# Kernel tuning notes

Hardware: AMD Instinct MI355X
Metric: run time of the kernel (lower is better)

The kernel has to match this reference:

```python
import jax, jax.numpy as jnp
import numpy as np

NUM_HEADS = 16
INNER = 128      # per-head q/k dim
OUT = 128        # per-head v dim
D_MODEL = 1024
SEQ = 2048
MASK_SCALE = -1000000000.0  # ENSURE_MASKED_IS_ZERO


def setup_inputs() -> dict:
    key = jax.random.key(0)
    ks = jax.random.split(key, 8)
    scale = 1.0 / np.sqrt(D_MODEL)
    inputs = jax.random.normal(ks[0], (SEQ, D_MODEL), dtype=jnp.float32)
    sequence_mask = jax.random.bernoulli(ks[1], 0.5, (SEQ,))
    Wq = jax.random.normal(ks[2], (D_MODEL, NUM_HEADS * INNER), dtype=jnp.float32) * scale
    bq = jnp.zeros((NUM_HEADS * INNER,), dtype=jnp.float32)
    Wk = jax.random.normal(ks[3], (D_MODEL, NUM_HEADS * INNER), dtype=jnp.float32) * scale
    bk = jnp.zeros((NUM_HEADS * INNER,), dtype=jnp.float32)
    Wv = jax.random.normal(ks[4], (D_MODEL, NUM_HEADS * OUT), dtype=jnp.float32) * scale
    bv = jnp.zeros((NUM_HEADS * OUT,), dtype=jnp.float32)
    return {"inputs": inputs, "sequence_mask": sequence_mask,
            "Wq": Wq, "bq": bq, "Wk": Wk, "bk": bk, "Wv": Wv, "bv": bv}


def reference(inputs, sequence_mask, Wq, bq, Wk, bk, Wv, bv):
    S = inputs.shape[0]
    # Dense projections, then split heads; vmap(in_axes=1) in the original == head-major layout [H, S, D]
    q = (inputs @ Wq + bq).reshape(S, NUM_HEADS, INNER).transpose(1, 0, 2)
    k = (inputs @ Wk + bk).reshape(S, NUM_HEADS, INNER).transpose(1, 0, 2)
    v = (inputs @ Wv + bv).reshape(S, NUM_HEADS, OUT).transpose(1, 0, 2)
    # raw scores / sqrt(d_k)
    scores = jnp.einsum('hsd,htd->hst', q, k) / jnp.sqrt(jnp.float32(INNER))
    # Faithful to original: scores are MULTIPLIED by the mask matrix
    # mask = outer(m, m) * (-1e9): -1e9 where both positions True, 0 otherwise.
    mask = (sequence_mask[:, None] & sequence_mask[None, :]).astype(scores.dtype) * MASK_SCALE
    scores = scores * mask  # broadcast over head axis
    attn = jax.nn.softmax(scores, axis=-1)           # [H, S, S]
    out = jnp.einsum('hst,htd->hsd', attn, v)        # [H, S, OUT]
    return out.transpose(1, 0, 2).reshape(S, NUM_HEADS * OUT)
```

## Files before the change

### kernel.cpp

```cpp
#include <hip/hip_runtime.h>
#include <hip/hip_bf16.h>
#include <cfloat>
#include <math.h>

typedef __bf16 bf16;
typedef __bf16 bf16x4 __attribute__((ext_vector_type(4)));
typedef __bf16 bf16x8 __attribute__((ext_vector_type(8)));
typedef float  floatx4 __attribute__((ext_vector_type(4)));
typedef float  floatx2 __attribute__((ext_vector_type(2)));

#define SEQ 2048
#define DM  1024
#define NP  2048
#define CAP (1 << 20)
#define MARGIN 0.5f
#define LBUF 1024

__device__ __forceinline__ unsigned enc_f(float f) {
  unsigned b = __float_as_uint(f);
  return ((int)b >= 0) ? (b | 0x80000000u) : ~b;
}
__device__ __forceinline__ float dec_f(unsigned u) {
  return (u & 0x80000000u) ? __uint_as_float(u & 0x7fffffffu) : __uint_as_float(~u);
}

__global__ __launch_bounds__(256) void mask_prep(
    const void* __restrict__ mraw, int* __restrict__ maskw,
    int* __restrict__ midx, int* __restrict__ mc,
    int* __restrict__ gcount, float* __restrict__ sums,
    unsigned long long* __restrict__ keys, unsigned* __restrict__ gmin) {
  int t = threadIdx.x;
  if (blockIdx.x > 0) {
    int b = blockIdx.x - 1;
    for (int j = 0; j < 4; j++) {
      int i = b * 1024 + j * 256 + t;
      keys[i] = ~0ULL;
      gmin[i] = 0xFFFFFFFFu;
    }
    if (b == 0) for (int i = t; i < 2048; i += 256) sums[i] = 0.f;
    return;
  }
  __shared__ int flags;
  __shared__ int lmask[2048];
  if (t == 0) { flags = 0; *gcount = 0; }
  __syncthreads();
  const unsigned short* u16 = (const unsigned short*)mraw;
  const unsigned* u32 = (const unsigned*)mraw;
  int f = 0;
  for (int i = t; i < 1024; i += 256) {
    unsigned short v = u16[i];
    if (v != 0 && v != 0x3F80u) f |= 1;
    if ((i & 1) == 0 && v == 0x3F80u) f |= 2;
  }
  for (int i = t; i < 512; i += 256)
    if (u32[i] > 1u) f |= 4;
  if (f) atomicOr(&flags, f);
  __syncthreads();
  int fl = flags;
  int mode;
  if (!(fl & 1)) mode = (fl & 2) ? 2 : 3;
  else           mode = (fl & 4) ? 1 : 0;
  for (int s = t; s < SEQ; s += 256) {
    int m;
    if (mode == 0)      m = (((const int*)mraw)[s] != 0);
    else if (mode == 1) m = (((const unsigned char*)mraw)[s] != 0);
    else if (mode == 2) m = (u16[s] != 0);
    else                m = (((const float*)mraw)[s] != 0.0f);
    maskw[s] = m; lmask[s] = m;
  }
  __syncthreads();
  if (t < 64) {
    int base = 0;
    for (int c = 0; c < 32; c++) {
      int s = c * 64 + t;
      bool m = lmask[s] != 0;
      unsigned long long bal = __ballot(m);
      if (m) midx[base + __popcll(bal & ((1ULL << t) - 1ULL))] = s;
      base += __popcll(bal);
    }
    if (t == 0) *mc = base;
  }
}

__global__ __launch_bounds__(256) void split_x(
    const float* __restrict__ X,
    bf16* __restrict__ Xh, bf16* __restrict__ Xm) {
  int i = blockIdx.x * 256 + threadIdx.x;
  floatx4 v = *(const floatx4*)(X + (size_t)i * 4);
  bf16x4 hv, mv;
  #pragma unroll
  for (int j = 0; j < 4; j++) {
    float x = v[j];
    bf16 h = (bf16)x; float r1 = x - (float)h;
    hv[j] = h; mv[j] = (bf16)r1;
  }
  *(bf16x4*)(Xh + (size_t)i * 4) = hv;
  *(bf16x4*)(Xm + (size_t)i * 4) = mv;
}

__global__ __launch_bounds__(256) void split_w(
    const float* __restrict__ Wq, const float* __restrict__ Wk,
    const float* __restrict__ Wv,
    bf16* __restrict__ Tqh, bf16* __restrict__ Tqm,
    bf16* __restrict__ Tkh, bf16* __restrict__ Tkm,
    bf16* __restrict__ Tvh) {
  int z = blockIdx.z;
  const float* W = (z == 0) ? Wq : (z == 1) ? Wk : Wv;
  bf16* Th = (z == 0) ? Tqh : (z == 1) ? Tkh : Tvh;
  bf16* Tm = (z == 0) ? Tqm : Tkm;
  __shared__ float tile[32][33];
  int n0 = blockIdx.x * 32, k0 = blockIdx.y * 32;
  int t = threadIdx.x, r = t >> 3, c4 = (t & 7) * 4;
  floatx4 v = *(const floatx4*)(W + (size_t)(k0 + r) * NP + n0 + c4);
  tile[r][c4 + 0] = v[0]; tile[r][c4 + 1] = v[1];
  tile[r][c4 + 2] = v[2]; tile[r][c4 + 3] = v[3];
  __syncthreads();
  bf16x4 hv, mv;
  #pragma unroll
  for (int j = 0; j < 4; j++) {
    float x = tile[c4 + j][r];
    bf16 h = (bf16)x; float r1 = x - (float)h;
    hv[j] = h; mv[j] = (bf16)r1;
  }
  size_t base = (size_t)(n0 + r) * DM + k0 + c4;
  *(bf16x4*)(Th + base) = hv;
  if (z < 2)
    *(bf16x4*)(Tm + base) = mv;
}

__global__ __launch_bounds__(256) void proj_qk3(
    const bf16* __restrict__ Xh, const bf16* __restrict__ Xm,
    const bf16* __restrict__ Qh_, const bf16* __restrict__ Qm_,
    const bf16* __restrict__ Kh_, const bf16* __restrict__ Km_,
    const float* __restrict__ bq, const float* __restrict__ bk,
    const int* __restrict__ midx, const int* __restrict__ mc,
    float* __restrict__ qf, float* __restrict__ kf,
    bf16* __restrict__ qbf, bf16* __restrict__ kbf) {
  int mcv = *mc;
  int lin = blockIdx.x;
  int z    = lin & 1;
  int head = (lin >> 1) & 15;
  int ms   = (lin >> 5) * 64;
  if (mcv == 0 || ms >= mcv) return;
  const bf16* WTh = z ? Kh_ : Qh_;
  const bf16* WTm = z ? Km_ : Qm_;
  const float* bia = z ? bk : bq;
  float* outf = z ? kf : qf;
  bf16*  outb = z ? kbf : qbf;
  int ns = head * 128;
  __shared__ alignas(16) bf16 Ah[64][40], Am[64][40];
  __shared__ alignas(16) bf16 Bh[128][40], Bm[128][40];
  int t = threadIdx.x, w = t >> 6, lane = t & 63, l15 = lane & 15, qd = lane >> 4;
  int wm = (w & 1) * 32, wn = (w >> 1) * 64;
  int amr = t >> 2, akb = (t & 3) * 8;
  int bnr = t >> 1, bkb = (t & 1) * 16;
  int cr = ms + amr;
  size_t arow = (size_t)midx[cr < mcv ? cr : (mcv - 1)] * DM + akb;
  const bf16* xhp = Xh + arow;
  const bf16* xmp = Xm + arow;
  const bf16* bhp = WTh + (size_t)(ns + bnr) * DM + bkb;
  const bf16* bmp = WTm + (size_t)(ns + bnr) * DM + bkb;

  floatx4 acc[2][4];
  for (int i = 0; i < 2; i++)
    for (int j = 0; j < 4; j++) acc[i][j] = (floatx4){0.f, 0.f, 0.f, 0.f};

  bf16x8 pa[2], pb[4];
  pa[0] = *(const bf16x8*)(xhp);
  pa[1] = *(const bf16x8*)(xmp);
  pb[0] = *(const bf16x8*)(bhp);     pb[1] = *(const bf16x8*)(bhp + 8);
  pb[2] = *(const bf16x8*)(bmp);     pb[3] = *(const bf16x8*)(bmp + 8);

  for (int kt = 0; kt < DM; kt += 32) {
    __syncthreads();
    *(bf16x8*)&Ah[amr][akb] = pa[0];
    *(bf16x8*)&Am[amr][akb] = pa[1];
    *(bf16x8*)&Bh[bnr][bkb]     = pb[0];
    *(bf16x8*)&Bh[bnr][bkb + 8] = pb[1];
    *(bf16x8*)&Bm[bnr][bkb]     = pb[2];
    *(bf16x8*)&Bm[bnr][bkb + 8] = pb[3];
    __syncthreads();
    if (kt + 32 < DM) {
      int k2 = kt + 32;
      pa[0] = *(const bf16x8*)(xhp + k2);
      pa[1] = *(const bf16x8*)(xmp + k2);
      pb[0] = *(const bf16x8*)(bhp + k2);     pb[1] = *(const bf16x8*)(bhp + k2 + 8);
      pb[2] = *(const bf16x8*)(bmp + k2);     pb[3] = *(const bf16x8*)(bmp + k2 + 8);
    }
    bf16x8 fah[2], fam[2], fbh[4], fbm[4];
    #pragma unroll
    for (int i = 0; i < 2; i++) {
      fah[i] = *(const bf16x8*)&Ah[wm + i * 16 + l15][qd * 8];
      fam[i] = *(const bf16x8*)&Am[wm + i * 16 + l15][qd * 8];
    }
    #pragma unroll
    for (int j = 0; j < 4; j++) {
      fbh[j] = *(const bf16x8*)&Bh[wn + j * 16 + l15][qd * 8];
      fbm[j] = *(const bf16x8*)&Bm[wn + j * 16 + l15][qd * 8];
    }
    #pragma unroll
    for (int i = 0; i < 2; i++)
      #pragma unroll
      for (int j = 0; j < 4; j++) {
        floatx4 a = acc[i][j];
        a = __builtin_amdgcn_mfma_f32_16x16x32_bf16(fam[i], fbh[j], a, 0, 0, 0);
        a = __builtin_amdgcn_mfma_f32_16x16x32_bf16(fah[i], fbm[j], a, 0, 0, 0);
        a = __builtin_amdgcn_mfma_f32_16x16x32_bf16(fah[i], fbh[j], a, 0, 0, 0);
        acc[i][j] = a;
      }
  }
  #pragma unroll
  for (int i = 0; i < 2; i++)
    #pragma unroll
    for (int j = 0; j < 4; j++) {
      int col = wn + j * 16 + l15;
      float bb = bia[ns + col];
      #pragma unroll
      for (int r = 0; r < 4; r++) {
        int row = ms + wm + i * 16 + qd * 4 + r;
        float v = acc[i][j][r] + bb;
        size_t idx = ((size_t)head * SEQ + row) * 128 + col;
        outf[idx] = v;
        outb[idx] = (bf16)v;
      }
    }
}

__global__ __launch_bounds__(256) void proj_v_mfma(
    const bf16* __restrict__ Xh, const bf16* __restrict__ Wvh,
    const float* __restrict__ bia, float* __restrict__ out,
    float* __restrict__ sums) {
  __shared__ alignas(16) bf16 As[64][40];
  __shared__ alignas(16) bf16 Bs[128][40];
  __shared__ float colsum[128];
  int lin = blockIdx.x;
  int ns = (lin & 15) * 128;
  int ms = (lin >> 4) * 64;
  int t = threadIdx.x, w = t >> 6, lane = t & 63, l15 = lane & 15, qd = lane >> 4;
  int wm = (w & 1) * 32, wn = (w >> 1) * 64;
  int amr = t >> 2, akb = (t & 3) * 8;
  int bnr = t >> 1, bkb = (t & 1) * 16;
  if (t < 128) colsum[t] = 0.f;
  const bf16* ap = Xh  + (size_t)(ms + amr) * DM + akb;
  const bf16* bp = Wvh + (size_t)(ns + bnr) * DM + bkb;
  floatx4 acc[2][4];
  for (int i = 0; i < 2; i++)
    for (int j = 0; j < 4; j++) acc[i][j] = (floatx4){0.f, 0.f, 0.f, 0.f};

  bf16x8 pa, pb[2];
  pa    = *(const bf16x8*)(ap);
  pb[0] = *(const bf16x8*)(bp);  pb[1] = *(const bf16x8*)(bp + 8);

  for (int kt = 0; kt < DM; kt += 32) {
    __syncthreads();
    *(bf16x8*)&As[amr][akb]     = pa;
    *(bf16x8*)&Bs[bnr][bkb]     = pb[0];
    *(bf16x8*)&Bs[bnr][bkb + 8] = pb[1];
    __syncthreads();
    if (kt + 32 < DM) {
      int k2 = kt + 32;
      pa    = *(const bf16x8*)(ap + k2);
      pb[0] = *(const bf16x8*)(bp + k2);  pb[1] = *(const bf16x8*)(bp + k2 + 8);
    }
    bf16x8 af[2], bfr[4];
    #pragma unroll
    for (int i = 0; i < 2; i++) af[i]  = *(const bf16x8*)&As[wm + i * 16 + l15][qd * 8];
    #pragma unroll
    for (int j = 0; j < 4; j++) bfr[j] = *(const bf16x8*)&Bs[wn + j * 16 + l15][qd * 8];
    #pragma unroll
    for (int i = 0; i < 2; i++)
      #pragma unroll
      for (int j = 0; j < 4; j++)
        acc[i][j] = __builtin_amdgcn_mfma_f32_16x16x32_bf16(af[i], bfr[j], acc[i][j], 0, 0, 0);
  }
  float part[4] = {0.f, 0.f, 0.f, 0.f};
  for (int i = 0; i < 2; i++) {
    for (int j = 0; j < 4; j++) {
      int n = ns + wn + j * 16 + l15;
      float bb = bia[n];
      for (int r = 0; r < 4; r++) {
        int m = ms + wm + i * 16 + qd * 4 + r;
        float v = acc[i][j][r] + bb;
        out[(size_t)m * NP + n] = v;
        part[j] += v;
      }
    }
  }
  for (int j = 0; j < 4; j++)
    atomicAdd(&colsum[wn + j * 16 + l15], part[j]);
  __syncthreads();
  if (t < 128) atomicAdd(&sums[ns + t], colsum[t]);
}

__global__ __launch_bounds__(256) void scores_min(
    const bf16* __restrict__ Qb, const bf16* __restrict__ Kb,
    const int* __restrict__ mc,
    unsigned* __restrict__ gmin) {
  int mcv = *mc;
  int h = blockIdx.x, s0 = blockIdx.y * 64;
  if (s0 >= mcv) return;
  int ntiles = (mcv + 63) >> 6;
  int half = (ntiles + 1) >> 1;
  int tbeg = blockIdx.z * half;
  int tend = ntiles < tbeg + half ? ntiles : tbeg + half;
  if (tbeg >= tend) return;
  __shared__ float lmin[64][4];
  int t = threadIdx.x, w = t >> 6, lane = t & 63, l15 = lane & 15, qd = lane >> 4;
  const bf16* Qh = Qb + (size_t)h * SEQ * 128;
  const bf16* Kh = Kb + (size_t)h * SEQ * 128;
  bf16x8 af[4][4];
  #pragma unroll
  for (int ksp = 0; ksp < 4; ksp++)
    #pragma unroll
    for (int i = 0; i < 4; i++)
      af[ksp][i] = *(const bf16x8*)(Qh + (size_t)(s0 + i * 16 + l15) * 128 + ksp * 32 + qd * 8);
  const bf16* kb = Kh + (size_t)(w * 16 + l15) * 128 + qd * 8;
  float rmin[4][4];
  for (int i = 0; i < 4; i++)
    for (int r = 0; r < 4; r++) rmin[i][r] = INFINITY;
  bf16x8 pre[4];
  #pragma unroll
  for (int ksp = 0; ksp < 4; ksp++)
    pre[ksp] = *(const bf16x8*)(kb + (size_t)tbeg * 8192 + ksp * 32);

  for (int tt = tbeg; tt < tend; tt++) {
    bf16x8 cur[4];
    #pragma unroll
    for (int ksp = 0; ksp < 4; ksp++) cur[ksp] = pre[ksp];
    if (tt + 1 < tend) {
      #pragma unroll
      for (int ksp = 0; ksp < 4; ksp++)
        pre[ksp] = *(const bf16x8*)(kb + (size_t)(tt + 1) * 8192 + ksp * 32);
    }
    floatx4 acc[4];
    for (int i = 0; i < 4; i++) acc[i] = (floatx4){0.f, 0.f, 0.f, 0.f};
    #pragma unroll
    for (int ksp = 0; ksp < 4; ksp++)
      #pragma unroll
      for (int i = 0; i < 4; i++)
        acc[i] = __builtin_amdgcn_mfma_f32_16x16x32_bf16(af[ksp][i], cur[ksp], acc[i], 0, 0, 0);
    bool okc = (tt * 64 + w * 16 + l15) < mcv;
    for (int i = 0; i < 4; i++)
      for (int r = 0; r < 4; r++)
        rmin[i][r] = fminf(rmin[i][r], okc ? acc[i][r] : INFINITY);
  }
  for (int m = 1; m < 16; m <<= 1)
    for (int i = 0; i < 4; i++)
      for (int r = 0; r < 4; r++)
        rmin[i][r] = fminf(rmin[i][r], __shfl_xor(rmin[i][r], m));
  if (l15 == 0)
    for (int i = 0; i < 4; i++)
      for (int r = 0; r < 4; r++)
        lmin[i * 16 + qd * 4 + r][w] = rmin[i][r];
  __syncthreads();
  if (t < 64) {
    int row = s0 + t;
    if (row < mcv) {
      float cm = fminf(fminf(lmin[t][0], lmin[t][1]), fminf(lmin[t][2], lmin[t][3]));
      atomicMin(&gmin[h * 2048 + row], enc_f(cm));
    }
  }
}

__global__ __launch_bounds__(256) void scores_collect(
    const bf16* __restrict__ Qb, const bf16* __restrict__ Kb,
    const int* __restrict__ mc, const unsigned* __restrict__ gmin,
    unsigned* __restrict__ cand, int* __restrict__ gcount) {
  int mcv = *mc;
  int h = blockIdx.x, s0 = blockIdx.y * 64;
  if (s0 >= mcv) return;
  int ntiles = (mcv + 63) >> 6;
  int half = (ntiles + 1) >> 1;
  int tbeg = blockIdx.z * half;
  int tend = ntiles < tbeg + half ? ntiles : tbeg + half;
  if (tbeg >= tend) return;
  __shared__ unsigned lbuf[LBUF];
  __shared__ int lcount;
  __shared__ int gbase;
  int t = threadIdx.x, w = t >> 6, lane = t & 63, l15 = lane & 15, qd = lane >> 4;
  if (t == 0) lcount = 0;
  const bf16* Qh = Qb + (size_t)h * SEQ * 128;
  const bf16* Kh = Kb + (size_t)h * SEQ * 128;
  bf16x8 af[4][4];
  #pragma unroll
  for (int ksp = 0; ksp < 4; ksp++)
    #pragma unroll
    for (int i = 0; i < 4; i++)
      af[ksp][i] = *(const bf16x8*)(Qh + (size_t)(s0 + i * 16 + l15) * 128 + ksp * 32 + qd * 8);
  float fm[4][4];
  for (int i = 0; i < 4; i++)
    for (int r = 0; r < 4; r++) {
      int row = s0 + i * 16 + qd * 4 + r;
      fm[i][r] = (row < mcv) ? dec_f(gmin[h * 2048 + row]) + MARGIN : -INFINITY;
    }
  const bf16* kb = Kh + (size_t)(w * 16 + l15) * 128 + qd * 8;
  bf16x8 pre[4];
  #pragma unroll
  for (int ksp = 0; ksp < 4; ksp++)
    pre[ksp] = *(const bf16x8*)(kb + (size_t)tbeg * 8192 + ksp * 32);
  __syncthreads();

  for (int tt = tbeg; tt < tend; tt++) {
    bf16x8 cur[4];
    #pragma unroll
    for (int ksp = 0; ksp < 4; ksp++) cur[ksp] = pre[ksp];
    if (tt + 1 < tend) {
      #pragma unroll
      for (int ksp = 0; ksp < 4; ksp++)
        pre[ksp] = *(const bf16x8*)(kb + (size_t)(tt + 1) * 8192 + ksp * 32);
    }
    floatx4 acc[4];
    for (int i = 0; i < 4; i++) acc[i] = (floatx4){0.f, 0.f, 0.f, 0.f};
    #pragma unroll
    for (int ksp = 0; ksp < 4; ksp++)
      #pragma unroll
      for (int i = 0; i < 4; i++)
        acc[i] = __builtin_amdgcn_mfma_f32_16x16x32_bf16(af[ksp][i], cur[ksp], acc[i], 0, 0, 0);
    int tg = tt * 64 + w * 16 + l15;
    if (tg < mcv) {
      for (int i = 0; i < 4; i++)
        for (int r = 0; r < 4; r++) {
          if (acc[i][r] <= fm[i][r]) {
            int rr = i * 16 + qd * 4 + r;
            unsigned enc = ((unsigned)h << 22) | ((unsigned)(s0 + rr) << 11) | (unsigned)tg;
            int lp = atomicAdd(&lcount, 1);
            if (lp < LBUF) {
              lbuf[lp] = enc;
            } else {
              int pos = atomicAdd(gcount, 1);
              if (pos < CAP) cand[pos] = enc;
            }
          }
        }
    }
  }
  __syncthreads();
  int cnt = lcount; if (cnt > LBUF) cnt = LBUF;
  if (t == 0) gbase = atomicAdd(gcount, cnt);
  __syncthreads();
  int base = gbase;
  for (int i = t; i < cnt; i += 256) {
    int pos = base + i;
    if (pos < CAP) cand[pos] = lbuf[i];
  }
}

__global__ __launch_bounds__(256) void rescore(
    const float* __restrict__ Q, const float* __restrict__ K,
    const int* __restrict__ midx,
    const unsigned* __restrict__ cand, const int* __restrict__ gcount,
    unsigned long long* __restrict__ keys) {
  int wid  = (blockIdx.x * 256 + threadIdx.x) >> 6;
  int lane = threadIdx.x & 63;
  int nw = gridDim.x * 4;
  int n = *gcount; if (n > CAP) n = CAP;
  for (int c = wid; c < n; c += nw) {
    unsigned u = cand[c];
    int h = u >> 22, cs = (u >> 11) & 2047, ct = u & 2047;
    floatx2 qv = *(const floatx2*)(Q + ((size_t)h * SEQ + cs) * 128 + lane * 2);
    floatx2 kv = *(const floatx2*)(K + ((size_t)h * SEQ + ct) * 128 + lane * 2);
    double d = (double)qv[0] * (double)kv[0] + (double)qv[1] * (double)kv[1];
    for (int off = 32; off; off >>= 1) d += __shfl_down(d, off);
    if (lane == 0) {
      int sorig = midx[cs], torig = midx[ct];
      long long b = __double_as_longlong(d);
      unsigned long long ub = (b >= 0) ? ((unsigned long long)b | 0x8000000000000000ULL)
                                       : ~(unsigned long long)b;
      unsigned long long key = (ub & ~2047ULL) | (unsigned long long)torig;
      atomicMin(&keys[(size_t)h * SEQ + sorig], key);
    }
  }
}

__global__ __launch_bounds__(256) void assemble(
    const float* __restrict__ V, const float* __restrict__ sums,
    const int* __restrict__ mask, const unsigned long long* __restrict__ keys,
    float* __restrict__ out) {
  int idx = blockIdx.x * 256 + threadIdx.x;
  int s = idx >> 11, n = idx & 2047, h = n >> 7;
  float val;
  if (mask[s]) {
    int tt = (int)(keys[(size_t)h * SEQ + s] & 2047ULL);
    val = V[(size_t)tt * NP + n];
  } else {
    val = sums[n] * (1.0f / 2048.0f);
  }
  out[idx] = val;
}

extern "C" void kernel_launch(void* const* d_in, const int* in_sizes, int n_in,
                              void* d_out, int out_size, void* d_ws, size_t ws_size,
                              hipStream_t stream) {
  (void)in_sizes; (void)n_in; (void)out_size; (void)ws_size;
  const float* X    = (const float*)d_in[0];
  const void*  mraw = d_in[1];
  const float* Wq   = (const float*)d_in[2];
  const float* bq   = (const float*)d_in[3];
  const float* Wk   = (const float*)d_in[4];
  const float* bk   = (const float*)d_in[5];
  const float* Wv   = (const float*)d_in[6];
  const float* bv   = (const float*)d_in[7];

  char* ws = (char*)d_ws;
  float* qf  = (float*)ws;
  float* kf  = (float*)(ws + ((size_t)16 << 20));
  bf16*  qbf = (bf16*) (ws + ((size_t)32 << 20));
  bf16*  kbf = (bf16*) (ws + ((size_t)40 << 20));
  bf16* wqh = (bf16*)(ws + ((size_t)48 << 20));
  bf16* wqm = (bf16*)(ws + ((size_t)52 << 20));
  bf16* wkh = (bf16*)(ws + ((size_t)56 << 20));
  bf16* wkm = (bf16*)(ws + ((size_t)60 << 20));
  float* vf = (float*)(ws + ((size_t)48 << 20));
  unsigned* cand = (unsigned*)(ws + ((size_t)64 << 20));
  char* misc = ws + ((size_t)72 << 20);
  int*   maskw  = (int*)misc;
  int*   midx   = (int*)(misc + (8 << 10));
  int*   mc     = (int*)(misc + (16 << 10));
  int*   gcount = (int*)(misc + (16 << 10) + 64);
  float* sums   = (float*)(misc + (32 << 10));
  unsigned long long* keys = (unsigned long long*)(misc + (64 << 10));
  unsigned* gmin = (unsigned*)(misc + (320 << 10));
  bf16* xh  = (bf16*)(ws + ((size_t)73 << 20));
  bf16* xm  = (bf16*)(ws + ((size_t)77 << 20));
  bf16* tvh = (bf16*)(ws + ((size_t)85 << 20));
  float* out = (float*)d_out;

  mask_prep<<<33, 256, 0, stream>>>(mraw, maskw, midx, mc, gcount, sums, keys, gmin);
  split_x<<<2048, 256, 0, stream>>>(X, xh, xm);
  split_w<<<dim3(64, 32, 3), 256, 0, stream>>>(Wq, Wk, Wv, wqh, wqm, wkh, wkm, tvh);
  proj_qk3<<<1024, 256, 0, stream>>>(xh, xm, wqh, wqm, wkh, wkm,
                                     bq, bk, midx, mc, qf, kf, qbf, kbf);
  proj_v_mfma<<<512, 256, 0, stream>>>(xh, tvh, bv, vf, sums);
  scores_min<<<dim3(16, 32, 2), 256, 0, stream>>>(qbf, kbf, mc, gmin);
  scores_collect<<<dim3(16, 32, 2), 256, 0, stream>>>(qbf, kbf, mc, gmin, cand, gcount);
  rescore<<<512, 256, 0, stream>>>(qf, kf, midx, cand, gcount, keys);
  assemble<<<16384, 256, 0, stream>>>(vf, sums, maskw, keys, out);
}
```

Before: 223.4 us.

## Merge prep kernels and Q/K/V projections into single launches, vectorize assemble

Folds mask preparation, the X split and the weight split into one prep kernel dispatched by block index. It also merges the Q/K and V projection GEMMs into one launch that shares a shared-memory buffer. The V output buffer moves to a separate workspace region so the two projections cannot alias when they run together. The assemble kernel now handles four floats per thread with vector loads and stores. The aim is fewer launch gaps and better overlap of independent work, at the cost of a higher shared-memory footprint per block.

```diff
diff --git a/kernel.cpp b/kernel.cpp
--- a/kernel.cpp
+++ b/kernel.cpp
@@ -24,93 +24,93 @@
   return (u & 0x80000000u) ? __uint_as_float(u & 0x7fffffffu) : __uint_as_float(~u);
 }
 
-__global__ __launch_bounds__(256) void mask_prep(
-    const void* __restrict__ mraw, int* __restrict__ maskw,
-    int* __restrict__ midx, int* __restrict__ mc,
-    int* __restrict__ gcount, float* __restrict__ sums,
-    unsigned long long* __restrict__ keys, unsigned* __restrict__ gmin) {
-  int t = threadIdx.x;
-  if (blockIdx.x > 0) {
-    int b = blockIdx.x - 1;
-    for (int j = 0; j < 4; j++) {
-      int i = b * 1024 + j * 256 + t;
-      keys[i] = ~0ULL;
-      gmin[i] = 0xFFFFFFFFu;
-    }
-    if (b == 0) for (int i = t; i < 2048; i += 256) sums[i] = 0.f;
-    return;
-  }
-  __shared__ int flags;
-  __shared__ int lmask[2048];
-  if (t == 0) { flags = 0; *gcount = 0; }
-  __syncthreads();
-  const unsigned short* u16 = (const unsigned short*)mraw;
-  const unsigned* u32 = (const unsigned*)mraw;
-  int f = 0;
-  for (int i = t; i < 1024; i += 256) {
-    unsigned short v = u16[i];
-    if (v != 0 && v != 0x3F80u) f |= 1;
-    if ((i & 1) == 0 && v == 0x3F80u) f |= 2;
-  }
-  for (int i = t; i < 512; i += 256)
-    if (u32[i] > 1u) f |= 4;
-  if (f) atomicOr(&flags, f);
-  __syncthreads();
-  int fl = flags;
-  int mode;
-  if (!(fl & 1)) mode = (fl & 2) ? 2 : 3;
-  else           mode = (fl & 4) ? 1 : 0;
-  for (int s = t; s < SEQ; s += 256) {
-    int m;
-    if (mode == 0)      m = (((const int*)mraw)[s] != 0);
-    else if (mode == 1) m = (((const unsigned char*)mraw)[s] != 0);
-    else if (mode == 2) m = (u16[s] != 0);
-    else                m = (((const float*)mraw)[s] != 0.0f);
-    maskw[s] = m; lmask[s] = m;
-  }
-  __syncthreads();
-  if (t < 64) {
-    int base = 0;
-    for (int c = 0; c < 32; c++) {
-      int s = c * 64 + t;
-      bool m = lmask[s] != 0;
-      unsigned long long bal = __ballot(m);
-      if (m) midx[base + __popcll(bal & ((1ULL << t) - 1ULL))] = s;
-      base += __popcll(bal);
-    }
-    if (t == 0) *mc = base;
-  }
-}
-
-__global__ __launch_bounds__(256) void split_x(
-    const float* __restrict__ X,
-    bf16* __restrict__ Xh, bf16* __restrict__ Xm) {
-  int i = blockIdx.x * 256 + threadIdx.x;
-  floatx4 v = *(const floatx4*)(X + (size_t)i * 4);
-  bf16x4 hv, mv;
-  #pragma unroll
-  for (int j = 0; j < 4; j++) {
-    float x = v[j];
-    bf16 h = (bf16)x; float r1 = x - (float)h;
-    hv[j] = h; mv[j] = (bf16)r1;
-  }
-  *(bf16x4*)(Xh + (size_t)i * 4) = hv;
-  *(bf16x4*)(Xm + (size_t)i * 4) = mv;
-}
-
-__global__ __launch_bounds__(256) void split_w(
+__global__ __launch_bounds__(256) void prep(
+    const void* __restrict__ mraw, const float* __restrict__ X,
     const float* __restrict__ Wq, const float* __restrict__ Wk,
     const float* __restrict__ Wv,
+    int* __restrict__ maskw, int* __restrict__ midx, int* __restrict__ mc,
+    int* __restrict__ gcount, float* __restrict__ sums,
+    unsigned long long* __restrict__ keys, unsigned* __restrict__ gmin,
+    bf16* __restrict__ Xh, bf16* __restrict__ Xm,
     bf16* __restrict__ Tqh, bf16* __restrict__ Tqm,
     bf16* __restrict__ Tkh, bf16* __restrict__ Tkm,
     bf16* __restrict__ Tvh) {
-  int z = blockIdx.z;
+  int b = blockIdx.x, t = threadIdx.x;
+  if (b < 33) {
+    if (b > 0) {
+      int bb = b - 1;
+      for (int j = 0; j < 4; j++) {
+        int i = bb * 1024 + j * 256 + t;
+        keys[i] = ~0ULL;
+        gmin[i] = 0xFFFFFFFFu;
+      }
+      if (bb == 0) for (int i = t; i < 2048; i += 256) sums[i] = 0.f;
+      return;
+    }
+    __shared__ int flags;
+    __shared__ int lmask[2048];
+    if (t == 0) { flags = 0; *gcount = 0; }
+    __syncthreads();
+    const unsigned short* u16 = (const unsigned short*)mraw;
+    const unsigned* u32 = (const unsigned*)mraw;
+    int f = 0;
+    for (int i = t; i < 1024; i += 256) {
+      unsigned short v = u16[i];
+      if (v != 0 && v != 0x3F80u) f |= 1;
+      if ((i & 1) == 0 && v == 0x3F80u) f |= 2;
+    }
+    for (int i = t; i < 512; i += 256)
+      if (u32[i] > 1u) f |= 4;
+    if (f) atomicOr(&flags, f);
+    __syncthreads();
+    int fl = flags;
+    int mode;
+    if (!(fl & 1)) mode = (fl & 2) ? 2 : 3;
+    else           mode = (fl & 4) ? 1 : 0;
+    for (int s = t; s < SEQ; s += 256) {
+      int m;
+      if (mode == 0)      m = (((const int*)mraw)[s] != 0);
+      else if (mode == 1) m = (((const unsigned char*)mraw)[s] != 0);
+      else if (mode == 2) m = (u16[s] != 0);
+      else                m = (((const float*)mraw)[s] != 0.0f);
+      maskw[s] = m; lmask[s] = m;
+    }
+    __syncthreads();
+    if (t < 64) {
+      int base = 0;
+      for (int c = 0; c < 32; c++) {
+        int s = c * 64 + t;
+        bool m = lmask[s] != 0;
+        unsigned long long bal = __ballot(m);
+        if (m) midx[base + __popcll(bal & ((1ULL << t) - 1ULL))] = s;
+        base += __popcll(bal);
+      }
+      if (t == 0) *mc = base;
+    }
+    return;
+  }
+  if (b < 2081) {
+    int i = (b - 33) * 256 + t;
+    floatx4 v = *(const floatx4*)(X + (size_t)i * 4);
+    bf16x4 hv, mv;
+    #pragma unroll
+    for (int j = 0; j < 4; j++) {
+      float x = v[j];
+      bf16 h = (bf16)x; float r1 = x - (float)h;
+      hv[j] = h; mv[j] = (bf16)r1;
+    }
+    *(bf16x4*)(Xh + (size_t)i * 4) = hv;
+    *(bf16x4*)(Xm + (size_t)i * 4) = mv;
+    return;
+  }
+  int bb = b - 2081;
+  int z = bb >> 11, rem = bb & 2047;
+  int n0 = (rem & 63) * 32, k0 = (rem >> 6) * 32;
   const float* W = (z == 0) ? Wq : (z == 1) ? Wk : Wv;
   bf16* Th = (z == 0) ? Tqh : (z == 1) ? Tkh : Tvh;
   bf16* Tm = (z == 0) ? Tqm : Tkm;
   __shared__ float tile[32][33];
-  int n0 = blockIdx.x * 32, k0 = blockIdx.y * 32;
-  int t = threadIdx.x, r = t >> 3, c4 = (t & 7) * 4;
+  int r = t >> 3, c4 = (t & 7) * 4;
   floatx4 v = *(const floatx4*)(W + (size_t)(k0 + r) * NP + n0 + c4);
   tile[r][c4 + 0] = v[0]; tile[r][c4 + 1] = v[1];
   tile[r][c4 + 2] = v[2]; tile[r][c4 + 3] = v[3];
@@ -128,168 +128,167 @@
     *(bf16x4*)(Tm + base) = mv;
 }
 
-__global__ __launch_bounds__(256) void proj_qk3(
+__global__ __launch_bounds__(256) void proj_fused(
     const bf16* __restrict__ Xh, const bf16* __restrict__ Xm,
     const bf16* __restrict__ Qh_, const bf16* __restrict__ Qm_,
     const bf16* __restrict__ Kh_, const bf16* __restrict__ Km_,
+    const bf16* __restrict__ Wvh,
     const float* __restrict__ bq, const float* __restrict__ bk,
+    const float* __restrict__ bv,
     const int* __restrict__ midx, const int* __restrict__ mc,
     float* __restrict__ qf, float* __restrict__ kf,
-    bf16* __restrict__ qbf, bf16* __restrict__ kbf) {
-  int mcv = *mc;
+    bf16* __restrict__ qbf, bf16* __restrict__ kbf,
+    float* __restrict__ vf, float* __restrict__ sums) {
+  __shared__ alignas(16) char smem[30720];
   int lin = blockIdx.x;
-  int z    = lin & 1;
-  int head = (lin >> 1) & 15;
-  int ms   = (lin >> 5) * 64;
-  if (mcv == 0 || ms >= mcv) return;
-  const bf16* WTh = z ? Kh_ : Qh_;
-  const bf16* WTm = z ? Km_ : Qm_;
-  const float* bia = z ? bk : bq;
-  float* outf = z ? kf : qf;
-  bf16*  outb = z ? kbf : qbf;
-  int ns = head * 128;
-  __shared__ alignas(16) bf16 Ah[64][40], Am[64][40];
-  __shared__ alignas(16) bf16 Bh[128][40], Bm[128][40];
   int t = threadIdx.x, w = t >> 6, lane = t & 63, l15 = lane & 15, qd = lane >> 4;
   int wm = (w & 1) * 32, wn = (w >> 1) * 64;
   int amr = t >> 2, akb = (t & 3) * 8;
   int bnr = t >> 1, bkb = (t & 1) * 16;
-  int cr = ms + amr;
-  size_t arow = (size_t)midx[cr < mcv ? cr : (mcv - 1)] * DM + akb;
-  const bf16* xhp = Xh + arow;
-  const bf16* xmp = Xm + arow;
-  const bf16* bhp = WTh + (size_t)(ns + bnr) * DM + bkb;
-  const bf16* bmp = WTm + (size_t)(ns + bnr) * DM + bkb;
-
-  floatx4 acc[2][4];
-  for (int i = 0; i < 2; i++)
-    for (int j = 0; j < 4; j++) acc[i][j] = (floatx4){0.f, 0.f, 0.f, 0.f};
-
-  bf16x8 pa[2], pb[4];
-  pa[0] = *(const bf16x8*)(xhp);
-  pa[1] = *(const bf16x8*)(xmp);
-  pb[0] = *(const bf16x8*)(bhp);     pb[1] = *(const bf16x8*)(bhp + 8);
-  pb[2] = *(const bf16x8*)(bmp);     pb[3] = *(const bf16x8*)(bmp + 8);
-
-  for (int kt = 0; kt < DM; kt += 32) {
+  if (lin < 1024) {
+    int mcv = *mc;
+    int z    = lin & 1;
+    int head = (lin >> 1) & 15;
+    int ms   = (lin >> 5) * 64;
+    if (mcv == 0 || ms >= mcv) return;
+    const bf16* WTh = z ? Kh_ : Qh_;
+    const bf16* WTm = z ? Km_ : Qm_;
+    const float* bia = z ? bk : bq;
+    float* outf = z ? kf : qf;
+    bf16*  outb = z ? kbf : qbf;
+    int ns = head * 128;
+    bf16 (*Ah)[40] = (bf16(*)[40])(smem);
+    bf16 (*Am)[40] = (bf16(*)[40])(smem + 5120);
+    bf16 (*Bh)[40] = (bf16(*)[40])(smem + 10240);
+    bf16 (*Bm)[40] = (bf16(*)[40])(smem + 20480);
+    int cr = ms + amr;
+    size_t arow = (size_t)midx[cr < mcv ? cr : (mcv - 1)] * DM + akb;
+    const bf16* xhp = Xh + arow;
+    const bf16* xmp = Xm + arow;
+    const bf16* bhp = WTh + (size_t)(ns + bnr) * DM + bkb;
+    const bf16* bmp = WTm + (size_t)(ns + bnr) * DM + bkb;
+
+    floatx4 acc[2][4];
+    for (int i = 0; i < 2; i++)
+      for (int j = 0; j < 4; j++) acc[i][j] = (floatx4){0.f, 0.f, 0.f, 0.f};
+
+    bf16x8 pa[2], pb[4];
+    pa[0] = *(const bf16x8*)(xhp);
+    pa[1] = *(const bf16x8*)(xmp);
+    pb[0] = *(const bf16x8*)(bhp);     pb[1] = *(const bf16x8*)(bhp + 8);
+    pb[2] = *(const bf16x8*)(bmp);     pb[3] = *(const bf16x8*)(bmp + 8);
+
+    for (int kt = 0; kt < DM; kt += 32) {
+      __syncthreads();
+      *(bf16x8*)&Ah[amr][akb] = pa[0];
+      *(bf16x8*)&Am[amr][akb] = pa[1];
+      *(bf16x8*)&Bh[bnr][bkb]     = pb[0];
+      *(bf16x8*)&Bh[bnr][bkb + 8] = pb[1];
+      *(bf16x8*)&Bm[bnr][bkb]     = pb[2];
+      *(bf16x8*)&Bm[bnr][bkb + 8] = pb[3];
+      __syncthreads();
+      if (kt + 32 < DM) {
+        int k2 = kt + 32;
+        pa[0] = *(const bf16x8*)(xhp + k2);
+        pa[1] = *(const bf16x8*)(xmp + k2);
+        pb[0] = *(const bf16x8*)(bhp + k2);     pb[1] = *(const bf16x8*)(bhp + k2 + 8);
+        pb[2] = *(const bf16x8*)(bmp + k2);     pb[3] = *(const bf16x8*)(bmp + k2 + 8);
+      }
+      bf16x8 fah[2], fam[2], fbh[4], fbm[4];
+      #pragma unroll
+      for (int i = 0; i < 2; i++) {
+        fah[i] = *(const bf16x8*)&Ah[wm + i * 16 + l15][qd * 8];
+        fam[i] = *(const bf16x8*)&Am[wm + i * 16 + l15][qd * 8];
+      }
+      #pragma unroll
+      for (int j = 0; j < 4; j++) {
+        fbh[j] = *(const bf16x8*)&Bh[wn + j * 16 + l15][qd * 8];
+        fbm[j] = *(const bf16x8*)&Bm[wn + j * 16 + l15][qd * 8];
+      }
+      #pragma unroll
+      for (int i = 0; i < 2; i++)
+        #pragma unroll
+        for (int j = 0; j < 4; j++) {
+          floatx4 a = acc[i][j];
+          a = __builtin_amdgcn_mfma_f32_16x16x32_bf16(fam[i], fbh[j], a, 0, 0, 0);
+          a = __builtin_amdgcn_mfma_f32_16x16x32_bf16(fah[i], fbm[j], a, 0, 0, 0);
+          a = __builtin_amdgcn_mfma_f32_16x16x32_bf16(fah[i], fbh[j], a, 0, 0, 0);
+          acc[i][j] = a;
+        }
+    }
+    #pragma unroll
+    for (int i = 0; i < 2; i++)
+      #pragma unroll
+      for (int j = 0; j < 4; j++) {
+        int col = wn + j * 16 + l15;
+        float bb = bia[ns + col];
+        #pragma unroll
+        for (int r = 0; r < 4; r++) {
+          int row = ms + wm + i * 16 + qd * 4 + r;
+          float v = acc[i][j][r] + bb;
+          size_t idx = ((size_t)head * SEQ + row) * 128 + col;
+          outf[idx] = v;
+          outb[idx] = (bf16)v;
+        }
+      }
+  } else {
+    int lin2 = lin - 1024;
+    int ns = (lin2 & 15) * 128;
+    int ms = (lin2 >> 4) * 64;
+    bf16 (*As)[40] = (bf16(*)[40])(smem);
+    bf16 (*Bs)[40] = (bf16(*)[40])(smem + 5120);
+    float* colsum = (float*)(smem + 15360);
+    if (t < 128) colsum[t] = 0.f;
+    const bf16* ap = Xh  + (size_t)(ms + amr) * DM + akb;
+    const bf16* bp = Wvh + (size_t)(ns + bnr) * DM + bkb;
+    floatx4 acc[2][4];
+    for (int i = 0; i < 2; i++)
+      for (int j = 0; j < 4; j++) acc[i][j] = (floatx4){0.f, 0.f, 0.f, 0.f};
+
+    bf16x8 pa, pb[2];
+    pa    = *(const bf16x8*)(ap);
+    pb[0] = *(const bf16x8*)(bp);  pb[1] = *(const bf16x8*)(bp + 8);
+
+    for (int kt = 0; kt < DM; kt += 32) {
+      __syncthreads();
+      *(bf16x8*)&As[amr][akb]     = pa;
+      *(bf16x8*)&Bs[bnr][bkb]     = pb[0];
+      *(bf16x8*)&Bs[bnr][bkb + 8] = pb[1];
+      __syncthreads();
+      if (kt + 32 < DM) {
+        int k2 = kt + 32;
+        pa    = *(const bf16x8*)(ap + k2);
+        pb[0] = *(const bf16x8*)(bp + k2);  pb[1] = *(const bf16x8*)(bp + k2 + 8);
+      }
+      bf16x8 af[2], bfr[4];
+      #pragma unroll
+      for (int i = 0; i < 2; i++) af[i]  = *(const bf16x8*)&As[wm + i * 16 + l15][qd * 8];
+      #pragma unroll
+      for (int j = 0; j < 4; j++) bfr[j] = *(const bf16x8*)&Bs[wn + j * 16 + l15][qd * 8];
+      #pragma unroll
+      for (int i = 0; i < 2; i++)
+        #pragma unroll
+        for (int j = 0; j < 4; j++)
+          acc[i][j] = __builtin_amdgcn_mfma_f32_16x16x32_bf16(af[i], bfr[j], acc[i][j], 0, 0, 0);
+    }
+    float part[4] = {0.f, 0.f, 0.f, 0.f};
+    for (int i = 0; i < 2; i++) {
+      for (int j = 0; j < 4; j++) {
+        int n = ns + wn + j * 16 + l15;
+        float bb = bv[n];
+        for (int r = 0; r < 4; r++) {
+          int m = ms + wm + i * 16 + qd * 4 + r;
+          float v = acc[i][j][r] + bb;
+          vf[(size_t)m * NP + n] = v;
+          part[j] += v;
+        }
+      }
+    }
+    for (int j = 0; j < 4; j++)
+      atomicAdd(&colsum[wn + j * 16 + l15], part[j]);
     __syncthreads();
-    *(bf16x8*)&Ah[amr][akb] = pa[0];
-    *(bf16x8*)&Am[amr][akb] = pa[1];
-    *(bf16x8*)&Bh[bnr][bkb]     = pb[0];
-    *(bf16x8*)&Bh[bnr][bkb + 8] = pb[1];
-    *(bf16x8*)&Bm[bnr][bkb]     = pb[2];
-    *(bf16x8*)&Bm[bnr][bkb + 8] = pb[3];
-    __syncthreads();
-    if (kt + 32 < DM) {
-      int k2 = kt + 32;
-      pa[0] = *(const bf16x8*)(xhp + k2);
-      pa[1] = *(const bf16x8*)(xmp + k2);
-      pb[0] = *(const bf16x8*)(bhp + k2);     pb[1] = *(const bf16x8*)(bhp + k2 + 8);
-      pb[2] = *(const bf16x8*)(bmp + k2);     pb[3] = *(const bf16x8*)(bmp + k2 + 8);
-    }
-    bf16x8 fah[2], fam[2], fbh[4], fbm[4];
-    #pragma unroll
-    for (int i = 0; i < 2; i++) {
-      fah[i] = *(const bf16x8*)&Ah[wm + i * 16 + l15][qd * 8];
-      fam[i] = *(const bf16x8*)&Am[wm + i * 16 + l15][qd * 8];
-    }
-    #pragma unroll
-    for (int j = 0; j < 4; j++) {
-      fbh[j] = *(const bf16x8*)&Bh[wn + j * 16 + l15][qd * 8];
-      fbm[j] = *(const bf16x8*)&Bm[wn + j * 16 + l15][qd * 8];
-    }
-    #pragma unroll
-    for (int i = 0; i < 2; i++)
-      #pragma unroll
-      for (int j = 0; j < 4; j++) {
-        floatx4 a = acc[i][j];
-        a = __builtin_amdgcn_mfma_f32_16x16x32_bf16(fam[i], fbh[j], a, 0, 0, 0);
-        a = __builtin_amdgcn_mfma_f32_16x16x32_bf16(fah[i], fbm[j], a, 0, 0, 0);
-        a = __builtin_amdgcn_mfma_f32_16x16x32_bf16(fah[i], fbh[j], a, 0, 0, 0);
-        acc[i][j] = a;
-      }
-  }
-  #pragma unroll
-  for (int i = 0; i < 2; i++)
-    #pragma unroll
-    for (int j = 0; j < 4; j++) {
-      int col = wn + j * 16 + l15;
-      float bb = bia[ns + col];
-      #pragma unroll
-      for (int r = 0; r < 4; r++) {
-        int row = ms + wm + i * 16 + qd * 4 + r;
-        float v = acc[i][j][r] + bb;
-        size_t idx = ((size_t)head * SEQ + row) * 128 + col;
-        outf[idx] = v;
-        outb[idx] = (bf16)v;
-      }
-    }
-}
-
-__global__ __launch_bounds__(256) void proj_v_mfma(
-    const bf16* __restrict__ Xh, const bf16* __restrict__ Wvh,
-    const float* __restrict__ bia, float* __restrict__ out,
-    float* __restrict__ sums) {
-  __shared__ alignas(16) bf16 As[64][40];
-  __shared__ alignas(16) bf16 Bs[128][40];
-  __shared__ float colsum[128];
-  int lin = blockIdx.x;
-  int ns = (lin & 15) * 128;
-  int ms = (lin >> 4) * 64;
-  int t = threadIdx.x, w = t >> 6, lane = t & 63, l15 = lane & 15, qd = lane >> 4;
-  int wm = (w & 1) * 32, wn = (w >> 1) * 64;
-  int amr = t >> 2, akb = (t & 3) * 8;
-  int bnr = t >> 1, bkb = (t & 1) * 16;
-  if (t < 128) colsum[t] = 0.f;
-  const bf16* ap = Xh  + (size_t)(ms + amr) * DM + akb;
-  const bf16* bp = Wvh + (size_t)(ns + bnr) * DM + bkb;
-  floatx4 acc[2][4];
-  for (int i = 0; i < 2; i++)
-    for (int j = 0; j < 4; j++) acc[i][j] = (floatx4){0.f, 0.f, 0.f, 0.f};
-
-  bf16x8 pa, pb[2];
-  pa    = *(const bf16x8*)(ap);
-  pb[0] = *(const bf16x8*)(bp);  pb[1] = *(const bf16x8*)(bp + 8);
-
-  for (int kt = 0; kt < DM; kt += 32) {
-    __syncthreads();
-    *(bf16x8*)&As[amr][akb]     = pa;
-    *(bf16x8*)&Bs[bnr][bkb]     = pb[0];
-    *(bf16x8*)&Bs[bnr][bkb + 8] = pb[1];
-    __syncthreads();
-    if (kt + 32 < DM) {
-      int k2 = kt + 32;
-      pa    = *(const bf16x8*)(ap + k2);
-      pb[0] = *(const bf16x8*)(bp + k2);  pb[1] = *(const bf16x8*)(bp + k2 + 8);
-    }
-    bf16x8 af[2], bfr[4];
-    #pragma unroll
-    for (int i = 0; i < 2; i++) af[i]  = *(const bf16x8*)&As[wm + i * 16 + l15][qd * 8];
-    #pragma unroll
-    for (int j = 0; j < 4; j++) bfr[j] = *(const bf16x8*)&Bs[wn + j * 16 + l15][qd * 8];
-    #pragma unroll
-    for (int i = 0; i < 2; i++)
-      #pragma unroll
-      for (int j = 0; j < 4; j++)
-        acc[i][j] = __builtin_amdgcn_mfma_f32_16x16x32_bf16(af[i], bfr[j], acc[i][j], 0, 0, 0);
-  }
-  float part[4] = {0.f, 0.f, 0.f, 0.f};
-  for (int i = 0; i < 2; i++) {
-    for (int j = 0; j < 4; j++) {
-      int n = ns + wn + j * 16 + l15;
-      float bb = bia[n];
-      for (int r = 0; r < 4; r++) {
-        int m = ms + wm + i * 16 + qd * 4 + r;
-        float v = acc[i][j][r] + bb;
-        out[(size_t)m * NP + n] = v;
-        part[j] += v;
-      }
-    }
-  }
-  for (int j = 0; j < 4; j++)
-    atomicAdd(&colsum[wn + j * 16 + l15], part[j]);
-  __syncthreads();
-  if (t < 128) atomicAdd(&sums[ns + t], colsum[t]);
+    if (t < 128) atomicAdd(&sums[ns + t], colsum[t]);
+  }
 }
 
 __global__ __launch_bounds__(256) void scores_min(
@@ -476,16 +475,18 @@
     const float* __restrict__ V, const float* __restrict__ sums,
     const int* __restrict__ mask, const unsigned long long* __restrict__ keys,
     float* __restrict__ out) {
-  int idx = blockIdx.x * 256 + threadIdx.x;
+  int q = blockIdx.x * 256 + threadIdx.x;
+  int idx = q * 4;
   int s = idx >> 11, n = idx & 2047, h = n >> 7;
-  float val;
+  floatx4 val;
   if (mask[s]) {
     int tt = (int)(keys[(size_t)h * SEQ + s] & 2047ULL);
-    val = V[(size_t)tt * NP + n];
+    val = *(const floatx4*)(V + (size_t)tt * NP + n);
   } else {
-    val = sums[n] * (1.0f / 2048.0f);
-  }
-  out[idx] = val;
+    floatx4 sv = *(const floatx4*)(sums + n);
+    for (int j = 0; j < 4; j++) val[j] = sv[j] * (1.0f / 2048.0f);
+  }
+  *(floatx4*)(out + idx) = val;
 }
 
 extern "C" void kernel_launch(void* const* d_in, const int* in_sizes, int n_in,
@@ -525,14 +526,16 @@
   bf16* tvh = (bf16*)(ws + ((size_t)85 << 20));
   float* out = (float*)d_out;
 
-  mask_prep<<<33, 256, 0, stream>>>(mraw, maskw, midx, mc, gcount, sums, keys, gmin);
-  split_x<<<2048, 256, 0, stream>>>(X, xh, xm);
-  split_w<<<dim3(64, 32, 3), 256, 0, stream>>>(Wq, Wk, Wv, wqh, wqm, wkh, wkm, tvh);
-  proj_qk3<<<1024, 256, 0, stream>>>(xh, xm, wqh, wqm, wkh, wkm,
-                                     bq, bk, midx, mc, qf, kf, qbf, kbf);
-  proj_v_mfma<<<512, 256, 0, stream>>>(xh, tvh, bv, vf, sums);
+  vf = (float*)(ws + ((size_t)89 << 20));
+
+  prep<<<8225, 256, 0, stream>>>(mraw, X, Wq, Wk, Wv,
+                                 maskw, midx, mc, gcount, sums, keys, gmin,
+                                 xh, xm, wqh, wqm, wkh, wkm, tvh);
+  proj_fused<<<1536, 256, 0, stream>>>(xh, xm, wqh, wqm, wkh, wkm, tvh,
+                                       bq, bk, bv, midx, mc,
+                                       qf, kf, qbf, kbf, vf, sums);
   scores_min<<<dim3(16, 32, 2), 256, 0, stream>>>(qbf, kbf, mc, gmin);
   scores_collect<<<dim3(16, 32, 2), 256, 0, stream>>>(qbf, kbf, mc, gmin, cand, gcount);
   rescore<<<512, 256, 0, stream>>>(qf, kf, midx, cand, gcount, keys);
-  assemble<<<16384, 256, 0, stream>>>(vf, sums, maskw, keys, out);
-}
+  assemble<<<4096, 256, 0, stream>>>(vf, sums, maskw, keys, out);
+}
```

Result: faster. 210.7 us (-5.7%).
